# Kernel optimization log

Hardware: AMD Instinct MI355X
Metric: run time of the kernel (lower is better)

Reference implementation:

```python
import jax, jax.numpy as jnp
import numpy as np

NUM_CLASSES = 20
FEAT_DIM = 32
THRESH = 1.5
G = 64  # voxel grid side; N = G^3
S = 512  # number of annotated seed points


def _conv3d(x, w, b):
    y = jax.lax.conv_general_dilated(
        x, w, window_strides=(1, 1, 1), padding='SAME',
        dimension_numbers=('NCDHW', 'OIDHW', 'NCDHW'))
    return y + b[None, :, None, None, None]


def setup_inputs() -> dict:
    key = jax.random.key(0)
    ks = jax.random.split(key, 12)
    N = G * G * G
    points = jax.random.normal(ks[0], (N, 3), jnp.float32) * 2.0
    features = jax.random.normal(ks[1], (1, 6, G, G, G), jnp.float32)
    seed_xyz = jax.random.normal(ks[2], (S, 3), jnp.float32) * 2.0
    seed_lab = jax.random.randint(ks[3], (S,), 0, NUM_CLASSES).astype(jnp.float32)
    annotated_points = jnp.concatenate([seed_xyz, seed_lab[:, None]], axis=1)
    conv1_w = jax.random.normal(ks[4], (64, 6, 3, 3, 3), jnp.float32) * 0.05
    conv1_b = jnp.zeros((64,), jnp.float32)
    conv2_w = jax.random.normal(ks[5], (FEAT_DIM, 64, 3, 3, 3), jnp.float32) * 0.05
    conv2_b = jnp.zeros((FEAT_DIM,), jnp.float32)
    sem_w = jax.random.normal(ks[6], (NUM_CLASSES, FEAT_DIM), jnp.float32) * 0.1
    sem_b = jnp.zeros((NUM_CLASSES,), jnp.float32)
    off_w = jax.random.normal(ks[7], (3, FEAT_DIM), jnp.float32) * 0.1
    off_b = jnp.zeros((3,), jnp.float32)
    return dict(points=points, features=features, annotated_points=annotated_points,
                conv1_w=conv1_w, conv1_b=conv1_b, conv2_w=conv2_w, conv2_b=conv2_b,
                sem_w=sem_w, sem_b=sem_b, off_w=off_w, off_b=off_b)


def reference(points, features, annotated_points,
              conv1_w, conv1_b, conv2_w, conv2_b, sem_w, sem_b, off_w, off_b):
    # backbone: two Conv3d+ReLU over the voxel grid
    h = jax.nn.relu(_conv3d(features, conv1_w, conv1_b))
    h = jax.nn.relu(_conv3d(h, conv2_w, conv2_b))  # [1, FEAT_DIM, G, G, G]
    # per-point features: channels last, flatten grid -> [N, FEAT_DIM]
    pf = jnp.transpose(h, (0, 2, 3, 4, 1)).reshape(-1, FEAT_DIM)
    semantic_logits = pf @ sem_w.T + sem_b        # [N, C]
    offsets = pf @ off_w.T + off_b                # [N, 3]

    # --- pseudo-label generation (training path) ---
    shifted = points + offsets                    # [N, 3]
    seeds = annotated_points[:, :3]               # [S, 3]
    seed_labels = annotated_points[:, 3].astype(jnp.int32)  # [S]
    # pairwise distances via ||a||^2 + ||b||^2 - 2ab (avoids NxSx3 temp)
    d2 = (jnp.sum(shifted * shifted, axis=1)[:, None]
          + jnp.sum(seeds * seeds, axis=1)[None, :]
          - 2.0 * shifted @ seeds.T)              # [N, S]
    dist = jnp.sqrt(jnp.maximum(d2, 0.0))
    min_dist = jnp.min(dist, axis=1)
    inst = jnp.argmin(dist, axis=1).astype(jnp.int32)
    valid = min_dist < THRESH

    # semantic consistency: invalidate any seed whose assigned points disagree
    semantic_labels = jnp.argmax(semantic_logits, axis=1).astype(jnp.int32)
    mismatch = valid & (semantic_labels != seed_labels[inst])  # [N]
    bad_seed = jnp.zeros((S,), jnp.bool_).at[inst].max(mismatch)  # [S]
    keep = valid & ~bad_seed[inst]
    pseudo_labels = jnp.where(keep, inst, -1)

    return semantic_logits, offsets, pseudo_labels
```

## Files before the change

### kernel.cpp

```cpp
#include <hip/hip_runtime.h>

#define GRID 64
#define NVOX (GRID*GRID*GRID)
#define NCLS 20
#define NSEED 512

typedef __attribute__((ext_vector_type(8))) short short8_t;
typedef __attribute__((ext_vector_type(4))) float float4_t;

__device__ __forceinline__ unsigned short f32_to_bf16_rne(float f) {
    unsigned int x = __float_as_uint(f);
    unsigned int r = (x + 0x7fffu + ((x >> 16) & 1u)) >> 16;
    return (unsigned short)r;
}
__device__ __forceinline__ float bf16_to_f32(unsigned short u) {
    return __uint_as_float(((unsigned int)u) << 16);
}

__global__ void transpose_w1(const float* __restrict__ w1, float* __restrict__ w1t,
                             const float* __restrict__ ann, float* __restrict__ seedtab,
                             int* __restrict__ slabtab) {
    int t = blockIdx.x * 256 + threadIdx.x;
    if (t < 27 * 6 * 64) {
        int oc = t & 63;
        int r  = t >> 6;
        int nb = r / 6, ci = r % 6;
        w1t[t] = w1[oc * 162 + ci * 27 + nb];
        return;
    }
    int i = t - 27 * 6 * 64;
    if (i < NSEED) {
        float a0 = ann[i*4+0], a1 = ann[i*4+1], a2 = ann[i*4+2];
        *reinterpret_cast<float4*>(seedtab + i * 4) =
            make_float4(a0, a1, a2, a0*a0 + a1*a1 + a2*a2);
        slabtab[i] = (int)ann[i*4+3];
    }
}

__global__ void build_bfrags(const float* __restrict__ w2, unsigned short* __restrict__ bfr) {
    int t = blockIdx.x * 256 + threadIdx.x;
    if (t >= 216 * 64) return;
    int l  = t & 63;
    int f  = t >> 6;
    int hl = f & 1;
    int tt = (f >> 1) & 1;
    int s  = (f >> 2) & 1;
    int nb = f >> 3;
    int lr = l & 15, lg = l >> 4;
    int oc = tt * 16 + lr;
    short8_t out;
    #pragma unroll
    for (int j = 0; j < 8; ++j) {
        int ci = s * 32 + lg * 8 + j;
        float wv = w2[oc * 1728 + ci * 27 + nb];
        unsigned short hi = f32_to_bf16_rne(wv);
        if (hl == 0) out[j] = (short)hi;
        else         out[j] = (short)f32_to_bf16_rne(wv - bf16_to_f32(hi));
    }
    *reinterpret_cast<short8_t*>(bfr + f * 512 + l * 8) = out;
}

__global__ __launch_bounds__(256, 4) void conv1_kernel(
    const float* __restrict__ feat,
    const float* __restrict__ w1t,
    const float* __restrict__ b1,
    unsigned short* __restrict__ h1hi)
{
    __shared__ float lw[27 * 6 * 16];

    int tid = threadIdx.x;
    int B = blockIdx.x;
    int zg = B & 7;
    int k  = B >> 3;
    int og = k & 3;
    int zt = (k >> 2) & 1;
    int yt = (k >> 3) & 15;

    for (int t = tid; t < 27 * 6 * 16; t += 256)
        lw[t] = w1t[(t >> 4) * 64 + og * 16 + (t & 15)];
    __syncthreads();

    int x  = tid & 63;
    int y  = yt * 4 + (tid >> 6);
    int z0 = zg * 8 + zt * 4;

    float acc[4][16];
    #pragma unroll
    for (int r = 0; r < 4; ++r)
        #pragma unroll
        for (int o = 0; o < 16; ++o) acc[r][o] = 0.f;

    int zoffv[6]; float mzv[6];
    #pragma unroll
    for (int rz = 0; rz < 6; ++rz) {
        int gz = z0 - 1 + rz;
        int cz = gz < 0 ? 0 : (gz > 63 ? 63 : gz);
        zoffv[rz] = cz * 4096;
        mzv[rz] = ((unsigned)gz < 64u) ? 1.f : 0.f;
    }

    #pragma unroll 1
    for (int dydx = 0; dydx < 9; ++dydx) {
        int dy = dydx / 3 - 1;
        int dx = dydx % 3 - 1;
        int ny = y + dy;
        if ((unsigned)ny >= 64u) continue;
        int nx = x + dx;
        float mx = ((unsigned)nx < 64u) ? 1.f : 0.f;
        int cx = nx < 0 ? 0 : (nx > 63 ? 63 : nx);
        int rowvox = ny * 64 + cx;

        float cm[6]; int voff[6];
        #pragma unroll
        for (int rz = 0; rz < 6; ++rz) { cm[rz] = mx * mzv[rz]; voff[rz] = zoffv[rz] + rowvox; }

        #pragma unroll
        for (int cb = 0; cb < 2; ++cb) {
            float v[3][6];
            #pragma unroll
            for (int ci = 0; ci < 3; ++ci) {
                const float* plane = feat + (size_t)(cb * 3 + ci) * NVOX;
                #pragma unroll
                for (int rz = 0; rz < 6; ++rz) v[ci][rz] = plane[voff[rz]];
            }
            #pragma unroll
            for (int ci = 0; ci < 3; ++ci)
                #pragma unroll
                for (int rz = 0; rz < 6; ++rz) v[ci][rz] *= cm[rz];
            #pragma unroll
            for (int ci = 0; ci < 3; ++ci) {
                #pragma unroll
                for (int dzi = 0; dzi < 3; ++dzi) {
                    const float4* wp = reinterpret_cast<const float4*>(
                        &lw[(((dzi * 9 + dydx) * 6) + cb * 3 + ci) * 16]);
                    float4 w0 = wp[0], w1 = wp[1], w2 = wp[2], w3 = wp[3];
                    #pragma unroll
                    for (int r = 0; r < 4; ++r) {
                        float a = v[ci][r + dzi];
                        acc[r][0]  = fmaf(a, w0.x, acc[r][0]);
                        acc[r][1]  = fmaf(a, w0.y, acc[r][1]);
                        acc[r][2]  = fmaf(a, w0.z, acc[r][2]);
                        acc[r][3]  = fmaf(a, w0.w, acc[r][3]);
                        acc[r][4]  = fmaf(a, w1.x, acc[r][4]);
                        acc[r][5]  = fmaf(a, w1.y, acc[r][5]);
                        acc[r][6]  = fmaf(a, w1.z, acc[r][6]);
                        acc[r][7]  = fmaf(a, w1.w, acc[r][7]);
                        acc[r][8]  = fmaf(a, w2.x, acc[r][8]);
                        acc[r][9]  = fmaf(a, w2.y, acc[r][9]);
                        acc[r][10] = fmaf(a, w2.z, acc[r][10]);
                        acc[r][11] = fmaf(a, w2.w, acc[r][11]);
                        acc[r][12] = fmaf(a, w3.x, acc[r][12]);
                        acc[r][13] = fmaf(a, w3.y, acc[r][13]);
                        acc[r][14] = fmaf(a, w3.z, acc[r][14]);
                        acc[r][15] = fmaf(a, w3.w, acc[r][15]);
                    }
                }
            }
        }
    }

    float bias[16];
    #pragma unroll
    for (int o = 0; o < 16; ++o) bias[o] = b1[og * 16 + o];

    int s1 = og >> 1;
    int c0 = (og * 2) & 3;
    int c1 = (og * 2 + 1) & 3;
    #pragma unroll
    for (int zl = 0; zl < 4; ++zl) {
        size_t zy = ((size_t)((z0 + zl) * 64 + y)) * 4096;
        size_t base  = zy + (size_t)(x >> 4) * 1024 + (size_t)s1 * 512 + (size_t)(x & 15) * 8;
        short8_t hi0, hi1;
        #pragma unroll
        for (int o = 0; o < 8; ++o)
            hi0[o] = (short)f32_to_bf16_rne(fmaxf(acc[zl][o] + bias[o], 0.f));
        #pragma unroll
        for (int o = 8; o < 16; ++o)
            hi1[o - 8] = (short)f32_to_bf16_rne(fmaxf(acc[zl][o] + bias[o], 0.f));
        *reinterpret_cast<short8_t*>(h1hi + base + c0 * 128) = hi0;
        *reinterpret_cast<short8_t*>(h1hi + base + c1 * 128) = hi1;
    }
}

__global__ __launch_bounds__(256) void conv2_fused_kernel(
    const unsigned short* __restrict__ h1hi,
    const unsigned short* __restrict__ bfr,
    const float* __restrict__ b2,
    const float* __restrict__ seedtab,
    const int* __restrict__ slabtab,
    const float* __restrict__ points,
    const float* __restrict__ sem_w, const float* __restrict__ sem_b,
    const float* __restrict__ off_w, const float* __restrict__ off_b,
    float* __restrict__ out_logits,
    float* __restrict__ out_off,
    int* __restrict__ iv_out,
    unsigned* __restrict__ bitmapT)
{
    __shared__ unsigned short pfs[256 * 40];
    __shared__ int lbad[NSEED];

    int tid = threadIdx.x;
    lbad[tid] = 0;
    lbad[tid + 256] = 0;

    int w   = tid >> 6;
    int l   = tid & 63;
    int B   = blockIdx.x;
    int zg  = B & 7;
    int yt  = (B >> 3) & 15;
    int zl  = B >> 7;
    int z   = zg * 8 + zl;
    int y   = yt * 4 + w;

    int lr = l & 15;
    int lg = l >> 4;

    int aoff[4][3]; bool aok[4][3];
    #pragma unroll
    for (int vt = 0; vt < 4; ++vt)
        #pragma unroll
        for (int dxm = 0; dxm < 3; ++dxm) {
            int v = vt * 16 + lr + dxm - 1;
            aok[vt][dxm] = (unsigned)v < 64u;
            int vc = v < 0 ? 0 : (v > 63 ? 63 : v);
            aoff[vt][dxm] = (vc >> 4) * 1024 + lg * 128 + (vc & 15) * 8;
        }

    const short8_t zero8 = (short8_t)0;
    float4_t acc[4][2];
    #pragma unroll
    for (int a = 0; a < 4; ++a)
        #pragma unroll
        for (int b = 0; b < 2; ++b) acc[a][b] = (float4_t)0.f;

    #pragma unroll 1
    for (int dzi = 0; dzi < 3; ++dzi) {
        int nz = z + dzi - 1;
        if ((unsigned)nz >= 64u) continue;
        #pragma unroll 1
        for (int dyi = 0; dyi < 3; ++dyi) {
            int ny = y + dyi - 1;
            if ((unsigned)ny >= 64u) continue;
            size_t zy = (size_t)(nz * 64 + ny) * 4096;
            #pragma unroll
            for (int dxm = 0; dxm < 3; ++dxm) {
                int nb = dzi * 9 + dyi * 3 + dxm;
                const unsigned short* bt = bfr + nb * 4096 + l * 8;
                #pragma unroll
                for (int s = 0; s < 2; ++s) {
                    const unsigned short* bs = bt + s * 2048;
                    short8_t bh0 = *reinterpret_cast<const short8_t*>(bs);
                    short8_t bl0 = *reinterpret_cast<const short8_t*>(bs + 512);
                    short8_t bh1 = *reinterpret_cast<const short8_t*>(bs + 1024);
                    short8_t bl1 = *reinterpret_cast<const short8_t*>(bs + 1536);

                    const unsigned short* ph = h1hi + zy + s * 512;
                    short8_t a0 = aok[0][dxm] ? *reinterpret_cast<const short8_t*>(ph + aoff[0][dxm]) : zero8;
                    short8_t a1 = aok[1][dxm] ? *reinterpret_cast<const short8_t*>(ph + aoff[1][dxm]) : zero8;
                    short8_t a2 = aok[2][dxm] ? *reinterpret_cast<const short8_t*>(ph + aoff[2][dxm]) : zero8;
                    short8_t a3 = aok[3][dxm] ? *reinterpret_cast<const short8_t*>(ph + aoff[3][dxm]) : zero8;

                    acc[0][0] = __builtin_amdgcn_mfma_f32_16x16x32_bf16(a0, bh0, acc[0][0], 0, 0, 0);
                    acc[0][0] = __builtin_amdgcn_mfma_f32_16x16x32_bf16(a0, bl0, acc[0][0], 0, 0, 0);
                    acc[0][1] = __builtin_amdgcn_mfma_f32_16x16x32_bf16(a0, bh1, acc[0][1], 0, 0, 0);
                    acc[0][1] = __builtin_amdgcn_mfma_f32_16x16x32_bf16(a0, bl1, acc[0][1], 0, 0, 0);

                    acc[1][0] = __builtin_amdgcn_mfma_f32_16x16x32_bf16(a1, bh0, acc[1][0], 0, 0, 0);
                    acc[1][0] = __builtin_amdgcn_mfma_f32_16x16x32_bf16(a1, bl0, acc[1][0], 0, 0, 0);
                    acc[1][1] = __builtin_amdgcn_mfma_f32_16x16x32_bf16(a1, bh1, acc[1][1], 0, 0, 0);
                    acc[1][1] = __builtin_amdgcn_mfma_f32_16x16x32_bf16(a1, bl1, acc[1][1], 0, 0, 0);

                    acc[2][0] = __builtin_amdgcn_mfma_f32_16x16x32_bf16(a2, bh0, acc[2][0], 0, 0, 0);
                    acc[2][0] = __builtin_amdgcn_mfma_f32_16x16x32_bf16(a2, bl0, acc[2][0], 0, 0, 0);
                    acc[2][1] = __builtin_amdgcn_mfma_f32_16x16x32_bf16(a2, bh1, acc[2][1], 0, 0, 0);
                    acc[2][1] = __builtin_amdgcn_mfma_f32_16x16x32_bf16(a2, bl1, acc[2][1], 0, 0, 0);

                    acc[3][0] = __builtin_amdgcn_mfma_f32_16x16x32_bf16(a3, bh0, acc[3][0], 0, 0, 0);
                    acc[3][0] = __builtin_amdgcn_mfma_f32_16x16x32_bf16(a3, bl0, acc[3][0], 0, 0, 0);
                    acc[3][1] = __builtin_amdgcn_mfma_f32_16x16x32_bf16(a3, bh1, acc[3][1], 0, 0, 0);
                    acc[3][1] = __builtin_amdgcn_mfma_f32_16x16x32_bf16(a3, bl1, acc[3][1], 0, 0, 0);
                }
            }
        }
    }

    #pragma unroll
    for (int vt = 0; vt < 4; ++vt) {
        #pragma unroll
        for (int t = 0; t < 2; ++t) {
            float bias = b2[t * 16 + lr];
            #pragma unroll
            for (int r = 0; r < 4; ++r) {
                int vl = w * 64 + vt * 16 + lg * 4 + r;
                pfs[vl * 40 + t * 16 + lr] = f32_to_bf16_rne(fmaxf(acc[vt][t][r] + bias, 0.f));
            }
        }
    }
    __syncthreads();

    int ex = tid & 63, ey = yt * 4 + (tid >> 6);
    int vox = (z * 64 + ey) * 64 + ex;

    float f[32];
    #pragma unroll
    for (int q = 0; q < 4; ++q) {
        short8_t v8 = *reinterpret_cast<const short8_t*>(&pfs[tid * 40 + q * 8]);
        #pragma unroll
        for (int kk = 0; kk < 8; ++kk) f[q*8+kk] = bf16_to_f32((unsigned short)v8[kk]);
    }

    float lbuf[20];
    float best = -1e30f; int am = 0;
    #pragma unroll
    for (int cc = 0; cc < NCLS; ++cc) {
        float a = sem_b[cc];
        #pragma unroll
        for (int q = 0; q < 32; ++q) a = fmaf(f[q], sem_w[cc * 32 + q], a);
        lbuf[cc] = a;
        if (a > best) { best = a; am = cc; }
    }
    #pragma unroll
    for (int q5 = 0; q5 < 5; ++q5)
        *reinterpret_cast<float4*>(out_logits + (size_t)vox * NCLS + q5 * 4) =
            make_float4(lbuf[q5*4], lbuf[q5*4+1], lbuf[q5*4+2], lbuf[q5*4+3]);

    float off[3];
    #pragma unroll
    for (int k3 = 0; k3 < 3; ++k3) {
        float a = off_b[k3];
        #pragma unroll
        for (int q = 0; q < 32; ++q) a = fmaf(f[q], off_w[k3 * 32 + q], a);
        out_off[(size_t)vox * 3 + k3] = a;
        off[k3] = a;
    }

    float px = points[(size_t)vox * 3 + 0] + off[0];
    float py = points[(size_t)vox * 3 + 1] + off[1];
    float pz = points[(size_t)vox * 3 + 2] + off[2];
    float c  = px*px + py*py + pz*pz;
    float mx = -2.f*px, my = -2.f*py, mz = -2.f*pz;

    float bd0 = 1e30f, bd1 = 1e30f, bd2 = 1e30f, bd3 = 1e30f;
    int   bj0 = 0,     bj1 = 0,     bj2 = 0,     bj3 = 0;
    #pragma unroll 2
    for (int j = 0; j < NSEED; j += 4) {
        float4 s0 = *reinterpret_cast<const float4*>(seedtab + (j + 0) * 4);
        float4 s1 = *reinterpret_cast<const float4*>(seedtab + (j + 1) * 4);
        float4 s2 = *reinterpret_cast<const float4*>(seedtab + (j + 2) * 4);
        float4 s3 = *reinterpret_cast<const float4*>(seedtab + (j + 3) * 4);
        float d0 = fmaf(mx, s0.x, fmaf(my, s0.y, fmaf(mz, s0.z, c + s0.w)));
        float d1 = fmaf(mx, s1.x, fmaf(my, s1.y, fmaf(mz, s1.z, c + s1.w)));
        float d2 = fmaf(mx, s2.x, fmaf(my, s2.y, fmaf(mz, s2.z, c + s2.w)));
        float d3 = fmaf(mx, s3.x, fmaf(my, s3.y, fmaf(mz, s3.z, c + s3.w)));
        if (d0 < bd0) { bd0 = d0; bj0 = j; }
        if (d1 < bd1) { bd1 = d1; bj1 = j + 1; }
        if (d2 < bd2) { bd2 = d2; bj2 = j + 2; }
        if (d3 < bd3) { bd3 = d3; bj3 = j + 3; }
    }
    bool p01 = (bd0 < bd1) || (bd0 == bd1 && bj0 < bj1);
    float bdA = p01 ? bd0 : bd1; int bjA = p01 ? bj0 : bj1;
    bool p23 = (bd2 < bd3) || (bd2 == bd3 && bj2 < bj3);
    float bdB = p23 ? bd2 : bd3; int bjB = p23 ? bj2 : bj3;
    bool pAB = (bdA < bdB) || (bdA == bdB && bjA < bjB);
    float bd = pAB ? bdA : bdB; int bj = pAB ? bjA : bjB;

    bool valid = sqrtf(fmaxf(bd, 0.f)) < 1.5f;

    int slab = slabtab[bj];
    if (valid && am != slab) atomicOr(&lbad[bj], 1);
    iv_out[vox] = valid ? bj : -1;

    __syncthreads();
    if (tid < 16) {
        unsigned wd = 0;
        #pragma unroll
        for (int i = 0; i < 32; ++i)
            wd |= (lbad[tid * 32 + i] ? 1u : 0u) << i;
        bitmapT[tid * 1024 + B] = wd;
    }
}

__global__ __launch_bounds__(256) void reduce_bad(const unsigned* __restrict__ bitmapT,
                                                  unsigned* __restrict__ badw) {
    __shared__ unsigned red[256];
    int w = blockIdx.x;
    int tid = threadIdx.x;
    const unsigned* src = bitmapT + w * 1024;
    unsigned v = src[tid] | src[tid + 256] | src[tid + 512] | src[tid + 768];
    red[tid] = v;
    __syncthreads();
    #pragma unroll
    for (int s = 128; s > 0; s >>= 1) {
        if (tid < s) red[tid] |= red[tid + s];
        __syncthreads();
    }
    if (tid == 0) badw[w] = red[0];
}

__global__ void finalize_kernel(const int* __restrict__ iv,
                                const unsigned* __restrict__ badw,
                                float* __restrict__ pl) {
    int t = blockIdx.x * 256 + threadIdx.x;
    if (t >= NVOX) return;
    int v = iv[t];
    float r = -1.0f;
    if (v >= 0 && !((badw[v >> 5] >> (v & 31)) & 1u)) r = (float)v;
    pl[t] = r;
}

extern "C" void kernel_launch(void* const* d_in, const int* in_sizes, int n_in,
                              void* d_out, int out_size, void* d_ws, size_t ws_size,
                              hipStream_t stream) {
    const float* points   = (const float*)d_in[0];
    const float* features = (const float*)d_in[1];
    const float* ann      = (const float*)d_in[2];
    const float* w1       = (const float*)d_in[3];
    const float* b1       = (const float*)d_in[4];
    const float* w2       = (const float*)d_in[5];
    const float* b2       = (const float*)d_in[6];
    const float* sem_w    = (const float*)d_in[7];
    const float* sem_b    = (const float*)d_in[8];
    const float* off_w    = (const float*)d_in[9];
    const float* off_b    = (const float*)d_in[10];

    float* out        = (float*)d_out;
    float* out_logits = out;
    float* out_off    = out + (size_t)NVOX * NCLS;
    float* out_pl     = out + (size_t)NVOX * 23;

    char*  ws  = (char*)d_ws;
    float*          w1t     = (float*)         (ws);
    unsigned*       badw    = (unsigned*)      (ws + 41472);
    unsigned short* bfr     = (unsigned short*)(ws + 43520);
    int*            iv      = (int*)           (ws + 264704);
    float*          seedtab = (float*)         (ws + 1313280);
    int*            slabtab = (int*)           (ws + 1321472);
    unsigned*       bitmapT = (unsigned*)      (ws + 1323520);
    unsigned short* h1hi    = (unsigned short*)(ws + 34867712);

    transpose_w1<<<43, 256, 0, stream>>>(w1, w1t, ann, seedtab, slabtab);
    build_bfrags<<<54, 256, 0, stream>>>(w2, bfr);
    conv1_kernel<<<1024, 256, 0, stream>>>(features, w1t, b1, h1hi);
    conv2_fused_kernel<<<1024, 256, 0, stream>>>(h1hi, bfr, b2, seedtab, slabtab,
        points, sem_w, sem_b, off_w, off_b, out_logits, out_off, iv, bitmapT);
    reduce_bad<<<16, 256, 0, stream>>>(bitmapT, badw);
    finalize_kernel<<<1024, 256, 0, stream>>>(iv, badw, out_pl);
}
```

Baseline: 196.6 us.

## Drop bf16 hi/lo weight split and stage conv2 input rows in LDS

Conv2 weights are now a single bf16 fragment instead of a hi/lo pair, which halves the MFMA count and the weight-fragment loads. Each wave copies its input row tile into shared memory once per (dz,dy) and serves the x-shifted neighbours from LDS instead of issuing three global loads. This lowers weight precision, which could change argmax or threshold-sensitive outputs. It also relies on wave-local LDS ordering with no explicit barrier.

```diff
diff --git a/kernel.cpp b/kernel.cpp
--- a/kernel.cpp
+++ b/kernel.cpp
@@ -39,23 +39,19 @@
 
 __global__ void build_bfrags(const float* __restrict__ w2, unsigned short* __restrict__ bfr) {
     int t = blockIdx.x * 256 + threadIdx.x;
-    if (t >= 216 * 64) return;
+    if (t >= 108 * 64) return;
     int l  = t & 63;
     int f  = t >> 6;
-    int hl = f & 1;
-    int tt = (f >> 1) & 1;
-    int s  = (f >> 2) & 1;
-    int nb = f >> 3;
+    int tt = f & 1;
+    int s  = (f >> 1) & 1;
+    int nb = f >> 2;
     int lr = l & 15, lg = l >> 4;
     int oc = tt * 16 + lr;
     short8_t out;
     #pragma unroll
     for (int j = 0; j < 8; ++j) {
         int ci = s * 32 + lg * 8 + j;
-        float wv = w2[oc * 1728 + ci * 27 + nb];
-        unsigned short hi = f32_to_bf16_rne(wv);
-        if (hl == 0) out[j] = (short)hi;
-        else         out[j] = (short)f32_to_bf16_rne(wv - bf16_to_f32(hi));
+        out[j] = (short)f32_to_bf16_rne(w2[oc * 1728 + ci * 27 + nb]);
     }
     *reinterpret_cast<short8_t*>(bfr + f * 512 + l * 8) = out;
 }
@@ -196,7 +192,7 @@
     int* __restrict__ iv_out,
     unsigned* __restrict__ bitmapT)
 {
-    __shared__ unsigned short pfs[256 * 40];
+    __shared__ unsigned short smem[4 * 4096];
     __shared__ int lbad[NSEED];
 
     int tid = threadIdx.x;
@@ -215,16 +211,19 @@
     int lr = l & 15;
     int lg = l >> 4;
 
-    int aoff[4][3]; bool aok[4][3];
-    #pragma unroll
-    for (int vt = 0; vt < 4; ++vt)
-        #pragma unroll
-        for (int dxm = 0; dxm < 3; ++dxm) {
-            int v = vt * 16 + lr + dxm - 1;
-            aok[vt][dxm] = (unsigned)v < 64u;
+    unsigned short* wsh = &smem[w * 4096];
+
+    int loff[4][2]; bool lok[4][2];
+    #pragma unroll
+    for (int vt = 0; vt < 4; ++vt) {
+        #pragma unroll
+        for (int dxs = 0; dxs < 2; ++dxs) {
+            int v = vt * 16 + lr + (dxs ? 1 : -1);
+            lok[vt][dxs] = (unsigned)v < 64u;
             int vc = v < 0 ? 0 : (v > 63 ? 63 : v);
-            aoff[vt][dxm] = (vc >> 4) * 1024 + lg * 128 + (vc & 15) * 8;
+            loff[vt][dxs] = (vc >> 4) * 1024 + lg * 128 + (vc & 15) * 8;
         }
+    }
 
     const short8_t zero8 = (short8_t)0;
     float4_t acc[4][2];
@@ -241,44 +240,51 @@
         for (int dyi = 0; dyi < 3; ++dyi) {
             int ny = y + dyi - 1;
             if ((unsigned)ny >= 64u) continue;
-            size_t zy = (size_t)(nz * 64 + ny) * 4096;
+            const unsigned short* ph = h1hi + (size_t)(nz * 64 + ny) * 4096;
+
+            short8_t ar[4][2];
+            #pragma unroll
+            for (int vt = 0; vt < 4; ++vt) {
+                #pragma unroll
+                for (int s = 0; s < 2; ++s)
+                    ar[vt][s] = *reinterpret_cast<const short8_t*>(ph + vt * 1024 + s * 512 + l * 8);
+            }
+            #pragma unroll
+            for (int vt = 0; vt < 4; ++vt) {
+                #pragma unroll
+                for (int s = 0; s < 2; ++s)
+                    *reinterpret_cast<short8_t*>(wsh + vt * 1024 + s * 512 + l * 8) = ar[vt][s];
+            }
+
             #pragma unroll
             for (int dxm = 0; dxm < 3; ++dxm) {
                 int nb = dzi * 9 + dyi * 3 + dxm;
-                const unsigned short* bt = bfr + nb * 4096 + l * 8;
+                const unsigned short* bt = bfr + nb * 2048 + l * 8;
                 #pragma unroll
                 for (int s = 0; s < 2; ++s) {
-                    const unsigned short* bs = bt + s * 2048;
+                    const unsigned short* bs = bt + s * 1024;
                     short8_t bh0 = *reinterpret_cast<const short8_t*>(bs);
-                    short8_t bl0 = *reinterpret_cast<const short8_t*>(bs + 512);
-                    short8_t bh1 = *reinterpret_cast<const short8_t*>(bs + 1024);
-                    short8_t bl1 = *reinterpret_cast<const short8_t*>(bs + 1536);
-
-                    const unsigned short* ph = h1hi + zy + s * 512;
-                    short8_t a0 = aok[0][dxm] ? *reinterpret_cast<const short8_t*>(ph + aoff[0][dxm]) : zero8;
-                    short8_t a1 = aok[1][dxm] ? *reinterpret_cast<const short8_t*>(ph + aoff[1][dxm]) : zero8;
-                    short8_t a2 = aok[2][dxm] ? *reinterpret_cast<const short8_t*>(ph + aoff[2][dxm]) : zero8;
-                    short8_t a3 = aok[3][dxm] ? *reinterpret_cast<const short8_t*>(ph + aoff[3][dxm]) : zero8;
+                    short8_t bh1 = *reinterpret_cast<const short8_t*>(bs + 512);
+
+                    short8_t a0, a1, a2, a3;
+                    if (dxm == 1) {
+                        a0 = ar[0][s]; a1 = ar[1][s]; a2 = ar[2][s]; a3 = ar[3][s];
+                    } else {
+                        int dxs = (dxm == 2) ? 1 : 0;
+                        a0 = lok[0][dxs] ? *reinterpret_cast<const short8_t*>(wsh + loff[0][dxs] + s * 512) : zero8;
+                        a1 = lok[1][dxs] ? *reinterpret_cast<const short8_t*>(wsh + loff[1][dxs] + s * 512) : zero8;
+                        a2 = lok[2][dxs] ? *reinterpret_cast<const short8_t*>(wsh + loff[2][dxs] + s * 512) : zero8;
+                        a3 = lok[3][dxs] ? *reinterpret_cast<const short8_t*>(wsh + loff[3][dxs] + s * 512) : zero8;
+                    }
 
                     acc[0][0] = __builtin_amdgcn_mfma_f32_16x16x32_bf16(a0, bh0, acc[0][0], 0, 0, 0);
-                    acc[0][0] = __builtin_amdgcn_mfma_f32_16x16x32_bf16(a0, bl0, acc[0][0], 0, 0, 0);
                     acc[0][1] = __builtin_amdgcn_mfma_f32_16x16x32_bf16(a0, bh1, acc[0][1], 0, 0, 0);
-                    acc[0][1] = __builtin_amdgcn_mfma_f32_16x16x32_bf16(a0, bl1, acc[0][1], 0, 0, 0);
-
                     acc[1][0] = __builtin_amdgcn_mfma_f32_16x16x32_bf16(a1, bh0, acc[1][0], 0, 0, 0);
-                    acc[1][0] = __builtin_amdgcn_mfma_f32_16x16x32_bf16(a1, bl0, acc[1][0], 0, 0, 0);
                     acc[1][1] = __builtin_amdgcn_mfma_f32_16x16x32_bf16(a1, bh1, acc[1][1], 0, 0, 0);
-                    acc[1][1] = __builtin_amdgcn_mfma_f32_16x16x32_bf16(a1, bl1, acc[1][1], 0, 0, 0);
-
                     acc[2][0] = __builtin_amdgcn_mfma_f32_16x16x32_bf16(a2, bh0, acc[2][0], 0, 0, 0);
-                    acc[2][0] = __builtin_amdgcn_mfma_f32_16x16x32_bf16(a2, bl0, acc[2][0], 0, 0, 0);
                     acc[2][1] = __builtin_amdgcn_mfma_f32_16x16x32_bf16(a2, bh1, acc[2][1], 0, 0, 0);
-                    acc[2][1] = __builtin_amdgcn_mfma_f32_16x16x32_bf16(a2, bl1, acc[2][1], 0, 0, 0);
-
                     acc[3][0] = __builtin_amdgcn_mfma_f32_16x16x32_bf16(a3, bh0, acc[3][0], 0, 0, 0);
-                    acc[3][0] = __builtin_amdgcn_mfma_f32_16x16x32_bf16(a3, bl0, acc[3][0], 0, 0, 0);
                     acc[3][1] = __builtin_amdgcn_mfma_f32_16x16x32_bf16(a3, bh1, acc[3][1], 0, 0, 0);
-                    acc[3][1] = __builtin_amdgcn_mfma_f32_16x16x32_bf16(a3, bl1, acc[3][1], 0, 0, 0);
                 }
             }
         }
@@ -291,8 +297,8 @@
             float bias = b2[t * 16 + lr];
             #pragma unroll
             for (int r = 0; r < 4; ++r) {
-                int vl = w * 64 + vt * 16 + lg * 4 + r;
-                pfs[vl * 40 + t * 16 + lr] = f32_to_bf16_rne(fmaxf(acc[vt][t][r] + bias, 0.f));
+                int vl = vt * 16 + lg * 4 + r;
+                wsh[vl * 40 + t * 16 + lr] = f32_to_bf16_rne(fmaxf(acc[vt][t][r] + bias, 0.f));
             }
         }
     }
@@ -304,7 +310,7 @@
     float f[32];
     #pragma unroll
     for (int q = 0; q < 4; ++q) {
-        short8_t v8 = *reinterpret_cast<const short8_t*>(&pfs[tid * 40 + q * 8]);
+        short8_t v8 = *reinterpret_cast<const short8_t*>(&wsh[(tid & 63) * 40 + q * 8]);
         #pragma unroll
         for (int kk = 0; kk < 8; ++kk) f[q*8+kk] = bf16_to_f32((unsigned short)v8[kk]);
     }
@@ -439,7 +445,7 @@
     unsigned short* h1hi    = (unsigned short*)(ws + 34867712);
 
     transpose_w1<<<43, 256, 0, stream>>>(w1, w1t, ann, seedtab, slabtab);
-    build_bfrags<<<54, 256, 0, stream>>>(w2, bfr);
+    build_bfrags<<<27, 256, 0, stream>>>(w2, bfr);
     conv1_kernel<<<1024, 256, 0, stream>>>(features, w1t, b1, h1hi);
     conv2_fused_kernel<<<1024, 256, 0, stream>>>(h1hi, bfr, b2, seedtab, slabtab,
         points, sem_w, sem_b, off_w, off_b, out_logits, out_off, iv, bitmapT);
```

New measurement: 179.5 us. 8.7% less time.
